# Optimization experiments

Measured on AMD Instinct MI355X. Metric: run time of the kernel, lower is better.

Reference implementation:

```python
import jax, jax.numpy as jnp
import numpy as np

TEMPERATURE = 0.7
REDUCTION = "mean"
MARGIN = 0.5  # the '+0.5' shift inside exp in the original


def setup_inputs() -> dict:
    key = jax.random.key(0)
    k1, k2 = jax.random.split(key)
    projection = jax.random.normal(k1, (8192, 256), dtype=jnp.float32)
    y = jax.random.randint(k2, (8192,), 0, 10, dtype=jnp.int64)
    return {"projection": projection, "y": y}


def reference(projection, y):
    # L2-normalize rows, cosine similarity matrix [n, n]
    n = projection.shape[0]
    proj = projection / jnp.linalg.norm(projection, axis=1, keepdims=True)
    sim = proj @ proj.T

    eq = (y[:, None] == y[None, :]).astype(sim.dtype)
    same = eq - jnp.eye(n, dtype=sim.dtype)   # same class, excluding self
    diff = 1.0 - eq                            # different class

    # Original per-row loop computes log(1 + sum_{j in diff, k in same}
    #   exp((sim[i,j] - sim[i,k] + 0.5)/t)) which separates as
    #   exp(0.5/t) * (sum_j exp(sim[i,j]/t)) * (sum_k exp(-sim[i,k]/t)).
    # Empty set -> the loop substitutes [0], i.e. that factor becomes exp(0)=1.
    A = jnp.sum(diff * jnp.exp(sim / TEMPERATURE), axis=1)
    B = jnp.sum(same * jnp.exp(-sim / TEMPERATURE), axis=1)
    A = jnp.where(jnp.sum(diff, axis=1) > 0, A, 1.0)
    B = jnp.where(jnp.sum(same, axis=1) > 0, B, 1.0)

    loss_per_row = jnp.log1p(jnp.exp(MARGIN / TEMPERATURE) * A * B)
    if REDUCTION == "mean":
        return jnp.mean(loss_per_row)
    return jnp.sum(loss_per_row)
```

## Files before the change

### kernel.cpp

```cpp
#include <hip/hip_runtime.h>
#include <hip/hip_bf16.h>


#define NF 256
#define TINV (1.0f / 0.7f)
#define SC2 2.0609929398439434f

typedef __attribute__((ext_vector_type(8))) short short8;
typedef __attribute__((ext_vector_type(4))) float float4v;

typedef const __attribute__((address_space(1))) unsigned int glb_u32;
typedef __attribute__((address_space(3))) unsigned int lds_u32;

__global__ __launch_bounds__(256)
void k_prep(const float* __restrict__ P, unsigned short* __restrict__ Pn,
            float* __restrict__ AB) {
    int wave = threadIdx.x >> 6, lane = threadIdx.x & 63;
    int row = blockIdx.x * 4 + wave;
    if (threadIdx.x < 8) AB[blockIdx.x * 8 + threadIdx.x] = 0.f;
    float4 v = *(const float4*)(P + (size_t)row * NF + lane * 4);
    float sq = v.x * v.x + v.y * v.y + v.z * v.z + v.w * v.w;
#pragma unroll
    for (int off = 32; off; off >>= 1) sq += __shfl_xor(sq, off, 64);
    float r = rsqrtf(sq);
    __hip_bfloat16 h0 = __float2bfloat16(v.x * r), h1 = __float2bfloat16(v.y * r),
                   h2 = __float2bfloat16(v.z * r), h3 = __float2bfloat16(v.w * r);
    ushort4 o = { *(unsigned short*)&h0, *(unsigned short*)&h1,
                  *(unsigned short*)&h2, *(unsigned short*)&h3 };
    *(ushort4*)(Pn + (size_t)row * NF + lane * 4) = o;
}

__global__ __launch_bounds__(256, 3)
void k_main(const unsigned short* __restrict__ Pn, const int* __restrict__ y,
            float* __restrict__ Aacc, float* __restrict__ Bacc) {
    __shared__ __align__(16) unsigned short Bs[64 * NF];
    __shared__ int yc[512];

    const int tid = threadIdx.x;
    const int I = blockIdx.x >> 4;
    const int G = blockIdx.x & 15;
    const int rb = I * 128, cb0 = G * 512;
    const int lane = tid & 63, wave = tid >> 6;
    const int quad = lane >> 4, l15 = lane & 15;

    yc[tid] = y[cb0 + tid];
    yc[256 + tid] = y[cb0 + 256 + tid];

    const unsigned short* pa = Pn + (size_t)(rb + wave * 32 + l15) * NF + quad * 8;
    short8 afr[2][8];
#pragma unroll
    for (int tr = 0; tr < 2; ++tr)
#pragma unroll
        for (int ks = 0; ks < 8; ++ks)
            afr[tr][ks] = *(const short8*)(pa + (size_t)tr * 16 * NF + ks * 32);

    unsigned yis[2];
#pragma unroll
    for (int tr = 0; tr < 2; ++tr) {
        int4 v = *(const int4*)(y + rb + wave * 32 + tr * 16 + quad * 4);
        yis[tr] = (unsigned)(v.x & 255) | ((unsigned)(v.y & 255) << 8) |
                  ((unsigned)(v.z & 255) << 16) | ((unsigned)(v.w & 255) << 24);
    }

    float rA[2][4], rB[2][4];
#pragma unroll
    for (int tr = 0; tr < 2; ++tr)
#pragma unroll
        for (int r = 0; r < 4; ++r) { rA[tr][r] = 0.f; rB[tr][r] = 0.f; }

#define DMA_CHUNK(c)                                                          \
    {                                                                         \
        _Pragma("unroll")                                                     \
        for (int i = 0; i < 8; ++i) {                                         \
            const int kc = wave * 8 + i;                                      \
            const unsigned short* src =                                       \
                Pn + (size_t)(cb0 + (c) * 64 + lane) * NF + kc * 8;           \
            __builtin_amdgcn_global_load_lds((glb_u32*)src,                   \
                (lds_u32*)&Bs[kc * 512], 16, 0, 0);                           \
        }                                                                     \
    }

    DMA_CHUNK(0)

#pragma unroll 1
    for (int c = 0; c < 8; ++c) {
        __syncthreads();

        float4v acc[2][4];
#pragma unroll
        for (int a = 0; a < 2; ++a)
#pragma unroll
            for (int b = 0; b < 4; ++b) acc[a][b] = (float4v){0.f, 0.f, 0.f, 0.f};

#pragma unroll
        for (int ks = 0; ks < 8; ++ks) {
            short8 fb[4];
#pragma unroll
            for (int tc = 0; tc < 4; ++tc)
                fb[tc] = *(const short8*)&Bs[(ks * 4 + quad) * 512 + (tc * 16 + l15) * 8];
#pragma unroll
            for (int tr = 0; tr < 2; ++tr)
#pragma unroll
                for (int tc = 0; tc < 4; ++tc)
                    acc[tr][tc] = __builtin_amdgcn_mfma_f32_16x16x32_bf16(
                        afr[tr][ks], fb[tc], acc[tr][tc], 0, 0, 0);
        }
        __syncthreads();
        if (c < 7) DMA_CHUNK(c + 1)

#pragma unroll
        for (int tc = 0; tc < 4; ++tc) {
            const int jl = c * 64 + tc * 16 + l15;
            const int yj = yc[jl];
            const int gj = cb0 + jl;
#pragma unroll
            for (int tr = 0; tr < 2; ++tr) {
                const int gi0 = rb + wave * 32 + tr * 16 + quad * 4;
#pragma unroll
                for (int r = 0; r < 4; ++r) {
                    const float s = acc[tr][tc][r];
                    const int cls = (yis[tr] >> (8 * r)) & 255;
                    const bool same = (cls == yj);
                    const float e = exp2f(s * (same ? -SC2 : SC2));
                    rA[tr][r] += same ? 0.f : e;
                    rB[tr][r] += (same && (gi0 + r != gj)) ? e : 0.f;
                }
            }
        }
    }

#pragma unroll
    for (int tr = 0; tr < 2; ++tr)
#pragma unroll
        for (int r = 0; r < 4; ++r) {
#pragma unroll
            for (int off = 1; off < 16; off <<= 1) {
                rA[tr][r] += __shfl_xor(rA[tr][r], off, 64);
                rB[tr][r] += __shfl_xor(rB[tr][r], off, 64);
            }
        }
    if (l15 == 0) {
#pragma unroll
        for (int tr = 0; tr < 2; ++tr)
#pragma unroll
            for (int r = 0; r < 4; ++r) {
                const int gi = rb + wave * 32 + tr * 16 + quad * 4 + r;
                atomicAdd(&Aacc[gi], rA[tr][r]);
                atomicAdd(&Bacc[gi], rB[tr][r]);
            }
    }
}

__global__ __launch_bounds__(1024)
void k_final(const float* __restrict__ Aacc, const float* __restrict__ Bacc,
             const int* __restrict__ y, float* __restrict__ out, int n) {
    __shared__ int hist[16];
    __shared__ float red[16];
    const int tid = threadIdx.x;
    if (tid < 16) hist[tid] = 0;
    __syncthreads();
    int loc[10];
#pragma unroll
    for (int cc = 0; cc < 10; ++cc) loc[cc] = 0;
    for (int i = tid; i < n; i += 1024) {
        const int yv = y[i];
#pragma unroll
        for (int cc = 0; cc < 10; ++cc) {
            unsigned long long m = __ballot(yv == cc);
            if ((tid & 63) == 0) loc[cc] += __popcll(m);
        }
    }
    if ((tid & 63) == 0)
#pragma unroll
        for (int cc = 0; cc < 10; ++cc) atomicAdd(&hist[cc], loc[cc]);
    __syncthreads();
    const float M = __expf(0.5f * TINV);
    float s = 0.f;
    for (int i = tid; i < n; i += 1024) {
        const int cc = hist[y[i] & 15];
        const float a = (n - cc) > 0 ? Aacc[i] : 1.0f;
        const float b = (cc - 1) > 0 ? Bacc[i] : 1.0f;
        s += log1pf(M * a * b);
    }
#pragma unroll
    for (int off = 32; off; off >>= 1) s += __shfl_xor(s, off, 64);
    if ((tid & 63) == 0) red[tid >> 6] = s;
    __syncthreads();
    if (tid == 0) {
        float t = 0.f;
#pragma unroll
        for (int w = 0; w < 16; ++w) t += red[w];
        out[0] = t / (float)n;
    }
}

extern "C" void kernel_launch(void* const* d_in, const int* in_sizes, int n_in,
                              void* d_out, int out_size, void* d_ws, size_t ws_size,
                              hipStream_t stream) {
    const float* P = (const float*)d_in[0];
    const int* y   = (const int*)d_in[1];
    float* out     = (float*)d_out;
    const int n = in_sizes[1];

    unsigned short* Pn = (unsigned short*)d_ws;
    float* Aacc = (float*)((char*)d_ws + (size_t)n * NF * 2);
    float* Bacc = Aacc + n;

    k_prep<<<n / 4, 256, 0, stream>>>(P, Pn, Aacc);
    k_main<<<(n / 128) * (n / 512), 256, 0, stream>>>(Pn, y, Aacc, Bacc);
    k_final<<<1, 1024, 0, stream>>>(Aacc, Bacc, y, out, n);
}
```

Baseline: 134.3 us.

## Exploit symmetry of similarity matrix to compute only lower-triangular tiles

Uses the symmetry of the cosine similarity matrix so each block computes only tiles at or below the diagonal. The blocks are laid out triangularly, and every product contributes to both its row and its column accumulators, with the column sums reduced in shared memory. This should roughly halve the MFMA and exp work. In exchange it adds cross-lane shuffles, shared and global atomics, and uneven per-block chunk counts near the diagonal.

Measured after the change: 173.0 us. +28.8%, slower.

```diff
diff --git a/kernel.cpp b/kernel.cpp
--- a/kernel.cpp
+++ b/kernel.cpp
@@ -34,17 +34,26 @@
 void k_main(const unsigned short* __restrict__ Pn, const int* __restrict__ y,
             float* __restrict__ Aacc, float* __restrict__ Bacc) {
     __shared__ __align__(16) unsigned short Bs[64 * NF];
-    __shared__ int yc[512];
+    __shared__ int yc[256];
+    __shared__ float colA[256], colB[256];
+
+    const int bid = blockIdx.x;
+    int a0 = (int)sqrtf((float)bid + 0.25f);
+    while (a0 * a0 + a0 > bid) --a0;
+    while ((a0 + 1) * (a0 + 1) + (a0 + 1) <= bid) ++a0;
+    int I, J;
+    const int so = (a0 + 1) * (a0 + 1);
+    if (bid < so) { I = 2 * a0;     J = bid - (a0 * a0 + a0); }
+    else          { I = 2 * a0 + 1; J = bid - so; }
+    const int rb = I * 128, cb0 = J * 256;
+    const int nc = min(4, (rb + 128 - cb0 + 63) >> 6);
 
     const int tid = threadIdx.x;
-    const int I = blockIdx.x >> 4;
-    const int G = blockIdx.x & 15;
-    const int rb = I * 128, cb0 = G * 512;
+    yc[tid] = y[cb0 + tid];
+    colA[tid] = 0.f; colB[tid] = 0.f;
+
     const int lane = tid & 63, wave = tid >> 6;
     const int quad = lane >> 4, l15 = lane & 15;
-
-    yc[tid] = y[cb0 + tid];
-    yc[256 + tid] = y[cb0 + 256 + tid];
 
     const unsigned short* pa = Pn + (size_t)(rb + wave * 32 + l15) * NF + quad * 8;
     short8 afr[2][8];
@@ -83,7 +92,7 @@
     DMA_CHUNK(0)
 
 #pragma unroll 1
-    for (int c = 0; c < 8; ++c) {
+    for (int c = 0; c < nc; ++c) {
         __syncthreads();
 
         float4v acc[2][4];
@@ -106,8 +115,9 @@
                         afr[tr][ks], fb[tc], acc[tr][tc], 0, 0, 0);
         }
         __syncthreads();
-        if (c < 7) DMA_CHUNK(c + 1)
-
+        if (c + 1 < nc) DMA_CHUNK(c + 1)
+
+        float cA[4] = {0.f, 0.f, 0.f, 0.f}, cB[4] = {0.f, 0.f, 0.f, 0.f};
 #pragma unroll
         for (int tc = 0; tc < 4; ++tc) {
             const int jl = c * 64 + tc * 16 + l15;
@@ -121,10 +131,27 @@
                     const float s = acc[tr][tc][r];
                     const int cls = (yis[tr] >> (8 * r)) & 255;
                     const bool same = (cls == yj);
+                    const bool valid = (gj < gi0 + r);
                     const float e = exp2f(s * (same ? -SC2 : SC2));
-                    rA[tr][r] += same ? 0.f : e;
-                    rB[tr][r] += (same && (gi0 + r != gj)) ? e : 0.f;
+                    const float ea = (valid && !same) ? e : 0.f;
+                    const float eb = (valid && same) ? e : 0.f;
+                    rA[tr][r] += ea; rB[tr][r] += eb;
+                    cA[tc] += ea;    cB[tc] += eb;
                 }
+            }
+        }
+#pragma unroll
+        for (int tc = 0; tc < 4; ++tc) {
+            cA[tc] += __shfl_xor(cA[tc], 16, 64);
+            cA[tc] += __shfl_xor(cA[tc], 32, 64);
+            cB[tc] += __shfl_xor(cB[tc], 16, 64);
+            cB[tc] += __shfl_xor(cB[tc], 32, 64);
+        }
+        if (quad == 0) {
+#pragma unroll
+            for (int tc = 0; tc < 4; ++tc) {
+                atomicAdd(&colA[c * 64 + tc * 16 + l15], cA[tc]);
+                atomicAdd(&colB[c * 64 + tc * 16 + l15], cB[tc]);
             }
         }
     }
@@ -148,6 +175,12 @@
                 atomicAdd(&Aacc[gi], rA[tr][r]);
                 atomicAdd(&Bacc[gi], rB[tr][r]);
             }
+    }
+
+    __syncthreads();
+    if (tid < nc * 64) {
+        atomicAdd(&Aacc[cb0 + tid], colA[tid]);
+        atomicAdd(&Bacc[cb0 + tid], colB[tid]);
     }
 }
 
@@ -207,6 +240,8 @@
     float* Bacc = Aacc + n;
 
     k_prep<<<n / 4, 256, 0, stream>>>(P, Pn, Aacc);
-    k_main<<<(n / 128) * (n / 512), 256, 0, stream>>>(Pn, y, Aacc, Bacc);
+    const int np = n / 128;
+    const int nblk = np * np / 4 + np / 2;
+    k_main<<<nblk, 256, 0, stream>>>(Pn, y, Aacc, Bacc);
     k_final<<<1, 1024, 0, stream>>>(Aacc, Bacc, y, out, n);
 }
```

## Halve column span per block, specialize diagonal tiles, parallelize final reduction

Applied to the files above, without the earlier changes.

The main kernel now gives each block 256 columns instead of 512, so twice as many blocks each run 4 chunks. Off-diagonal blocks skip the self-index check by summing the total and same-class terms and deriving A as their difference; only the block holding the diagonal does the index comparison. The final kernel is spread across n/256 blocks that combine through an atomic add into a zeroed output, instead of one 1024-thread block. This adds a memset, recomputes the histogram in every final block, and computing A as T−B may lose a little float precision.

Measured after the change: 153.1 us. +14.0%, slower.

```diff
diff --git a/kernel.cpp b/kernel.cpp
--- a/kernel.cpp
+++ b/kernel.cpp
@@ -34,17 +34,18 @@
 void k_main(const unsigned short* __restrict__ Pn, const int* __restrict__ y,
             float* __restrict__ Aacc, float* __restrict__ Bacc) {
     __shared__ __align__(16) unsigned short Bs[64 * NF];
-    __shared__ int yc[512];
+    __shared__ int yc[256];
 
     const int tid = threadIdx.x;
-    const int I = blockIdx.x >> 4;
-    const int G = blockIdx.x & 15;
-    const int rb = I * 128, cb0 = G * 512;
+    const int I = blockIdx.x >> 5;
+    const int g = blockIdx.x & 31;
+    const int rb = I * 128, cb0 = g * 256;
+    const bool diag = (g == (I >> 1));
+
+    yc[tid] = y[cb0 + tid];
+
     const int lane = tid & 63, wave = tid >> 6;
     const int quad = lane >> 4, l15 = lane & 15;
-
-    yc[tid] = y[cb0 + tid];
-    yc[256 + tid] = y[cb0 + 256 + tid];
 
     const unsigned short* pa = Pn + (size_t)(rb + wave * 32 + l15) * NF + quad * 8;
     short8 afr[2][8];
@@ -62,11 +63,11 @@
                   ((unsigned)(v.z & 255) << 16) | ((unsigned)(v.w & 255) << 24);
     }
 
-    float rA[2][4], rB[2][4];
+    float rT[2][4], rB[2][4];
 #pragma unroll
     for (int tr = 0; tr < 2; ++tr)
 #pragma unroll
-        for (int r = 0; r < 4; ++r) { rA[tr][r] = 0.f; rB[tr][r] = 0.f; }
+        for (int r = 0; r < 4; ++r) { rT[tr][r] = 0.f; rB[tr][r] = 0.f; }
 
 #define DMA_CHUNK(c)                                                          \
     {                                                                         \
@@ -83,7 +84,7 @@
     DMA_CHUNK(0)
 
 #pragma unroll 1
-    for (int c = 0; c < 8; ++c) {
+    for (int c = 0; c < 4; ++c) {
         __syncthreads();
 
         float4v acc[2][4];
@@ -106,24 +107,41 @@
                         afr[tr][ks], fb[tc], acc[tr][tc], 0, 0, 0);
         }
         __syncthreads();
-        if (c < 7) DMA_CHUNK(c + 1)
-
-#pragma unroll
-        for (int tc = 0; tc < 4; ++tc) {
-            const int jl = c * 64 + tc * 16 + l15;
-            const int yj = yc[jl];
-            const int gj = cb0 + jl;
-#pragma unroll
-            for (int tr = 0; tr < 2; ++tr) {
-                const int gi0 = rb + wave * 32 + tr * 16 + quad * 4;
-#pragma unroll
-                for (int r = 0; r < 4; ++r) {
-                    const float s = acc[tr][tc][r];
-                    const int cls = (yis[tr] >> (8 * r)) & 255;
-                    const bool same = (cls == yj);
-                    const float e = exp2f(s * (same ? -SC2 : SC2));
-                    rA[tr][r] += same ? 0.f : e;
-                    rB[tr][r] += (same && (gi0 + r != gj)) ? e : 0.f;
+        if (c < 3) DMA_CHUNK(c + 1)
+
+        if (!diag) {
+#pragma unroll
+            for (int tc = 0; tc < 4; ++tc) {
+                const int yj = yc[c * 64 + tc * 16 + l15];
+#pragma unroll
+                for (int tr = 0; tr < 2; ++tr)
+#pragma unroll
+                    for (int r = 0; r < 4; ++r) {
+                        const float s = acc[tr][tc][r];
+                        const bool same = (((yis[tr] >> (8 * r)) & 255) == (unsigned)yj);
+                        const float e = exp2f(s * (same ? -SC2 : SC2));
+                        rT[tr][r] += e;
+                        rB[tr][r] += same ? e : 0.f;
+                    }
+            }
+        } else {
+#pragma unroll
+            for (int tc = 0; tc < 4; ++tc) {
+                const int jl = c * 64 + tc * 16 + l15;
+                const int yj = yc[jl];
+                const int gj = cb0 + jl;
+#pragma unroll
+                for (int tr = 0; tr < 2; ++tr) {
+                    const int gi0 = rb + wave * 32 + tr * 16 + quad * 4;
+#pragma unroll
+                    for (int r = 0; r < 4; ++r) {
+                        const float s = acc[tr][tc][r];
+                        const bool same = (((yis[tr] >> (8 * r)) & 255) == (unsigned)yj);
+                        const bool ne = (gi0 + r != gj);
+                        const float e = exp2f(s * (same ? -SC2 : SC2));
+                        rT[tr][r] += ne ? e : 0.f;
+                        rB[tr][r] += (same && ne) ? e : 0.f;
+                    }
                 }
             }
         }
@@ -135,7 +153,7 @@
         for (int r = 0; r < 4; ++r) {
 #pragma unroll
             for (int off = 1; off < 16; off <<= 1) {
-                rA[tr][r] += __shfl_xor(rA[tr][r], off, 64);
+                rT[tr][r] += __shfl_xor(rT[tr][r], off, 64);
                 rB[tr][r] += __shfl_xor(rB[tr][r], off, 64);
             }
         }
@@ -145,53 +163,51 @@
 #pragma unroll
             for (int r = 0; r < 4; ++r) {
                 const int gi = rb + wave * 32 + tr * 16 + quad * 4 + r;
-                atomicAdd(&Aacc[gi], rA[tr][r]);
+                atomicAdd(&Aacc[gi], rT[tr][r] - rB[tr][r]);
                 atomicAdd(&Bacc[gi], rB[tr][r]);
             }
     }
 }
 
-__global__ __launch_bounds__(1024)
+__global__ __launch_bounds__(256)
 void k_final(const float* __restrict__ Aacc, const float* __restrict__ Bacc,
              const int* __restrict__ y, float* __restrict__ out, int n) {
     __shared__ int hist[16];
-    __shared__ float red[16];
+    __shared__ float red[4];
     const int tid = threadIdx.x;
+    const int i0 = blockIdx.x * 256 + tid;
+
     if (tid < 16) hist[tid] = 0;
     __syncthreads();
-    int loc[10];
-#pragma unroll
-    for (int cc = 0; cc < 10; ++cc) loc[cc] = 0;
-    for (int i = tid; i < n; i += 1024) {
-        const int yv = y[i];
-#pragma unroll
-        for (int cc = 0; cc < 10; ++cc) {
-            unsigned long long m = __ballot(yv == cc);
-            if ((tid & 63) == 0) loc[cc] += __popcll(m);
-        }
-    }
-    if ((tid & 63) == 0)
-#pragma unroll
-        for (int cc = 0; cc < 10; ++cc) atomicAdd(&hist[cc], loc[cc]);
+    {
+        int loc[10];
+#pragma unroll
+        for (int cc = 0; cc < 10; ++cc) loc[cc] = 0;
+        for (int i = tid; i < n; i += 256) {
+            const int yv = y[i];
+#pragma unroll
+            for (int cc = 0; cc < 10; ++cc) {
+                unsigned long long m = __ballot(yv == cc);
+                if ((tid & 63) == 0) loc[cc] += __popcll(m);
+            }
+        }
+        if ((tid & 63) == 0)
+#pragma unroll
+            for (int cc = 0; cc < 10; ++cc) atomicAdd(&hist[cc], loc[cc]);
+    }
     __syncthreads();
     const float M = __expf(0.5f * TINV);
-    float s = 0.f;
-    for (int i = tid; i < n; i += 1024) {
-        const int cc = hist[y[i] & 15];
-        const float a = (n - cc) > 0 ? Aacc[i] : 1.0f;
-        const float b = (cc - 1) > 0 ? Bacc[i] : 1.0f;
-        s += log1pf(M * a * b);
-    }
+    const int cc = hist[y[i0] & 15];
+    float a = Aacc[i0], b = Bacc[i0];
+    a = (n - cc) > 0 ? a : 1.0f;
+    b = (cc - 1) > 0 ? b : 1.0f;
+    float s = log1pf(M * a * b);
 #pragma unroll
     for (int off = 32; off; off >>= 1) s += __shfl_xor(s, off, 64);
     if ((tid & 63) == 0) red[tid >> 6] = s;
     __syncthreads();
-    if (tid == 0) {
-        float t = 0.f;
-#pragma unroll
-        for (int w = 0; w < 16; ++w) t += red[w];
-        out[0] = t / (float)n;
-    }
+    if (tid == 0)
+        atomicAdd(out, (red[0] + red[1] + red[2] + red[3]) / (float)n);
 }
 
 extern "C" void kernel_launch(void* const* d_in, const int* in_sizes, int n_in,
@@ -206,7 +222,8 @@
     float* Aacc = (float*)((char*)d_ws + (size_t)n * NF * 2);
     float* Bacc = Aacc + n;
 
+    hipMemsetAsync(out, 0, sizeof(float), stream);
     k_prep<<<n / 4, 256, 0, stream>>>(P, Pn, Aacc);
-    k_main<<<(n / 128) * (n / 512), 256, 0, stream>>>(Pn, y, Aacc, Bacc);
-    k_final<<<1, 1024, 0, stream>>>(Aacc, Bacc, y, out, n);
-}
+    k_main<<<(n / 128) * (n / 256), 256, 0, stream>>>(Pn, y, Aacc, Bacc);
+    k_final<<<n / 256, 256, 0, stream>>>(Aacc, Bacc, y, out, n);
+}
```
